# Kernel optimization log

Measured on AMD Instinct MI355X. Metric: run time of the kernel, lower is better.

The kernel has to match this reference:

```python
import jax, jax.numpy as jnp
import numpy as np

EPS = 1e-12
TAU = 1.0

def _normalize(x, axis=-1):
    # matches torch.nn.functional.normalize (p=2, eps=1e-12)
    n = jnp.linalg.norm(x, axis=axis, keepdims=True)
    return x / jnp.maximum(n, EPS)

def setup_inputs() -> dict:
    key = jax.random.key(0)
    ks = jax.random.split(key, 6)
    N, B, D, K = 8192, 512, 64, 4
    input_rating = jax.random.uniform(ks[0], (B, N), dtype=jnp.float32)
    # row-normalized-scale adjacency (mimics a normalized item-item graph)
    item_adj = jax.random.uniform(ks[1], (N, N), dtype=jnp.float32) * (2.0 / N)
    item_emb = jax.random.normal(ks[2], (N, D), dtype=jnp.float32) * float(np.sqrt(2.0 / (N + D)))
    proto_emb = jax.random.normal(ks[3], (K, D), dtype=jnp.float32) * float(np.sqrt(2.0 / (K + D)))
    enc_w = jax.random.normal(ks[4], (2 * D, N), dtype=jnp.float32) * float(np.sqrt(2.0 / (N + 2 * D)))
    enc_b = jax.random.normal(ks[5], (2 * D,), dtype=jnp.float32) * 0.01
    return {"input_rating": input_rating, "item_adj": item_adj, "item_emb": item_emb,
            "proto_emb": proto_emb, "enc_w": enc_w, "enc_b": enc_b}

def reference(input_rating, item_adj, item_emb, proto_emb, enc_w, enc_b):
    D = enc_b.shape[0] // 2
    prototypes = _normalize(proto_emb)          # [K, D]
    items = _normalize(item_emb)                # [N, D]
    cates = jax.nn.softmax(items @ prototypes.T / TAU, axis=-1)  # [N, K] (eval: mode branch)
    # per-prototype masked ratings, vectorized over K: [K, B, N]
    x_k = input_rating[None, :, :] * cates.T[:, None, :]
    x_k = _normalize(x_k)                       # fn.normalize(x_k, p=2) over items dim
    # two-hop propagation through dense item-item adjacency
    tmp = jnp.einsum('kbn,nm->kbm', x_k, item_adj)
    tmp = jnp.einsum('kbn,nm->kbm', tmp, item_adj)
    x = (tmp + x_k) / 2.0                       # dropout is identity in eval
    h = jnp.einsum('kbn,on->kbo', x, enc_w) + enc_b  # [K, B, 2D]
    mu = _normalize(h[..., :D])                 # [K, B, D]
    logvar = -h[..., D:]                        # [K, B, D]
    z = _normalize(mu)                          # eval: reparameterize returns mu
    logits_k = jnp.einsum('kbd,nd->kbn', z, items) / TAU
    probs = jnp.sum(jnp.exp(logits_k) * cates.T[:, None, :], axis=0)  # [B, N]
    logits = jnp.log(probs)
    return logits, mu, logvar
```

## Files before the change

kernel.cpp:

```cpp
#include <hip/hip_runtime.h>

typedef __attribute__((ext_vector_type(8))) short short8;
typedef __attribute__((ext_vector_type(4))) float f32x4;

#define AS3P(x) ((__attribute__((address_space(3))) void*)(x))
#define AS1P(x) ((const __attribute__((address_space(1))) void*)(x))

__device__ __forceinline__ unsigned short f2bf(float f) {
    unsigned int u = __float_as_uint(f);
    u += 0x7fffu + ((u >> 16) & 1u);
    return (unsigned short)(u >> 16);
}
__device__ __forceinline__ float bf2f(unsigned short b) {
    return __uint_as_float(((unsigned int)b) << 16);
}
__device__ __forceinline__ float waveReduceSum(float v) {
    #pragma unroll
    for (int off = 32; off; off >>= 1) v += __shfl_xor(v, off, 64);
    return v;
}

__global__ __launch_bounds__(256) void k_mega(const float* __restrict__ adj,
                                              unsigned short* __restrict__ adj_bf,
                                              const float* __restrict__ enc_w,
                                              unsigned short* __restrict__ encw,
                                              const float* __restrict__ item_emb,
                                              const float* __restrict__ proto,
                                              unsigned short* __restrict__ items_bf,
                                              float* __restrict__ catesT) {
    __shared__ float sp[256];
    int bx = blockIdx.x, tid = threadIdx.x;
    if (bx < 33280) {
        const float* src = (bx < 32768) ? adj : enc_w;
        unsigned short* dst = (bx < 32768) ? adj_bf : encw;
        size_t base = (bx < 32768) ? (size_t)bx : (size_t)(bx - 32768);
        size_t i = (base * 256 + tid) * 8;
        float4 a = *(const float4*)(src + i);
        float4 b = *(const float4*)(src + i + 4);
        uint4 pk;
        pk.x = (unsigned int)f2bf(a.x) | ((unsigned int)f2bf(a.y) << 16);
        pk.y = (unsigned int)f2bf(a.z) | ((unsigned int)f2bf(a.w) << 16);
        pk.z = (unsigned int)f2bf(b.x) | ((unsigned int)f2bf(b.y) << 16);
        pk.w = (unsigned int)f2bf(b.z) | ((unsigned int)f2bf(b.w) << 16);
        *(uint4*)(dst + i) = pk;
        return;
    }
    sp[tid] = proto[tid];
    __syncthreads();
    {
        float v = sp[tid];
        float ss = waveReduceSum(v * v);
        sp[tid] = v * (1.f / fmaxf(sqrtf(ss), 1e-12f));
    }
    __syncthreads();
    int i = (bx - 33280) * 256 + tid;
    const float4* row = (const float4*)(item_emb + (size_t)i * 64);
    float4 f[16];
    float ss = 0.f;
    #pragma unroll
    for (int q = 0; q < 16; ++q) {
        f[q] = row[q];
        ss += f[q].x * f[q].x + f[q].y * f[q].y + f[q].z * f[q].z + f[q].w * f[q].w;
    }
    float inv = 1.f / fmaxf(sqrtf(ss), 1e-12f);
    float dots[4] = {0.f, 0.f, 0.f, 0.f};
    unsigned short* ob = items_bf + (size_t)i * 64;
    #pragma unroll
    for (int q = 0; q < 16; ++q) {
        f[q].x *= inv; f[q].y *= inv; f[q].z *= inv; f[q].w *= inv;
        #pragma unroll
        for (int k = 0; k < 4; ++k) {
            dots[k] += f[q].x * sp[k * 64 + q * 4 + 0] + f[q].y * sp[k * 64 + q * 4 + 1]
                     + f[q].z * sp[k * 64 + q * 4 + 2] + f[q].w * sp[k * 64 + q * 4 + 3];
        }
    }
    #pragma unroll
    for (int q = 0; q < 16; q += 2) {
        uint4 pk;
        pk.x = (unsigned int)f2bf(f[q].x)     | ((unsigned int)f2bf(f[q].y) << 16);
        pk.y = (unsigned int)f2bf(f[q].z)     | ((unsigned int)f2bf(f[q].w) << 16);
        pk.z = (unsigned int)f2bf(f[q + 1].x) | ((unsigned int)f2bf(f[q + 1].y) << 16);
        pk.w = (unsigned int)f2bf(f[q + 1].z) | ((unsigned int)f2bf(f[q + 1].w) << 16);
        *(uint4*)(ob + q * 4) = pk;
    }
    float m = fmaxf(fmaxf(dots[0], dots[1]), fmaxf(dots[2], dots[3]));
    float e0 = expf(dots[0] - m), e1 = expf(dots[1] - m), e2 = expf(dots[2] - m), e3 = expf(dots[3] - m);
    float is = 1.f / (e0 + e1 + e2 + e3);
    catesT[0 * 8192 + i] = e0 * is;
    catesT[1 * 8192 + i] = e1 * is;
    catesT[2 * 8192 + i] = e2 * is;
    catesT[3 * 8192 + i] = e3 * is;
}

__global__ __launch_bounds__(256) void k_gemm_part(const unsigned short* __restrict__ A,
                                                   const unsigned short* __restrict__ B,
                                                   unsigned short* __restrict__ Cout,
                                                   int M, int ksplit, int lda, int ldb, int ldc) {
    __shared__ unsigned short lA[128 * 64];
    __shared__ unsigned short lB[128 * 64];
    int tid = threadIdx.x;
    int lane = tid & 63;
    int w = tid >> 6;
    int wr = w >> 1, wc = w & 1;
    int mBase = blockIdx.y * 128;
    int nBase = blockIdx.x * 128;
    int Kbeg = blockIdx.z * ksplit;
    int Kend = Kbeg + ksplit;

    f32x4 acc[4][4] = {};

    const unsigned short* Ablk = A + (size_t)mBase * lda;
    const unsigned short* Bblk = B + (size_t)nBase * ldb;
    int srow = tid >> 3;
    int scg = (tid & 7) ^ (srow & 7);
    char* ldsA_w = (char*)lA + w * 1024;
    char* ldsB_w = (char*)lB + w * 1024;

    for (int k0 = Kbeg; k0 < Kend; k0 += 64) {
        __syncthreads();
        #pragma unroll
        for (int it = 0; it < 4; ++it) {
            const unsigned short* ga = Ablk + (size_t)(it * 32 + srow) * lda + k0 + scg * 8;
            __builtin_amdgcn_global_load_lds(AS1P(ga), AS3P(ldsA_w + it * 4096), 16, 0, 0);
            const unsigned short* gb = Bblk + (size_t)(it * 32 + srow) * ldb + k0 + scg * 8;
            __builtin_amdgcn_global_load_lds(AS1P(gb), AS3P(ldsB_w + it * 4096), 16, 0, 0);
        }
        __syncthreads();
        #pragma unroll
        for (int kk = 0; kk < 2; ++kk) {
            short8 af[4], bfr[4];
            #pragma unroll
            for (int i = 0; i < 4; ++i) {
                int rowa = wr * 64 + i * 16 + (lane & 15);
                int slot = kk * 4 + (lane >> 4);
                af[i] = *(const short8*)((const char*)lA + rowa * 128 + ((slot ^ (rowa & 7)) * 16));
                int rowb = wc * 64 + i * 16 + (lane & 15);
                bfr[i] = *(const short8*)((const char*)lB + rowb * 128 + ((slot ^ (rowb & 7)) * 16));
            }
            #pragma unroll
            for (int i = 0; i < 4; ++i)
                #pragma unroll
                for (int j = 0; j < 4; ++j)
                    acc[i][j] = __builtin_amdgcn_mfma_f32_16x16x32_bf16(af[i], bfr[j], acc[i][j], 0, 0, 0);
        }
    }

    unsigned short* outP = Cout + (size_t)blockIdx.z * M * ldc;
    #pragma unroll
    for (int i = 0; i < 4; ++i) {
        int rbase = mBase + wr * 64 + i * 16 + (lane >> 4) * 4;
        #pragma unroll
        for (int j = 0; j < 4; ++j) {
            int col = nBase + wc * 64 + j * 16 + (lane & 15);
            #pragma unroll
            for (int r = 0; r < 4; ++r)
                outP[(size_t)(rbase + r) * ldc + col] = f2bf(acc[i][j][r]);
        }
    }
}

__global__ __launch_bounds__(256) void k_red1(const unsigned short* __restrict__ part,
                                              unsigned short* __restrict__ outT,
                                              const float* __restrict__ rating,
                                              const float* __restrict__ catesT,
                                              unsigned short* __restrict__ rating_bf,
                                              float* __restrict__ inv4) {
    __shared__ float t[64 * 129];
    int tid = threadIdx.x;
    if (blockIdx.x < 128) {
        int m0 = blockIdx.x * 64;
        #pragma unroll
        for (int j = 0; j < 4; ++j) {
            int f = tid + j * 256;
            int m = f >> 4, o = (f & 15) * 8;
            float a[8] = {0.f,0.f,0.f,0.f,0.f,0.f,0.f,0.f};
            #pragma unroll
            for (int sp = 0; sp < 16; ++sp) {
                const unsigned short* p = part + (size_t)sp * 8192 * 128 + (size_t)(m0 + m) * 128 + o;
                uint4 v = *(const uint4*)p;
                a[0] += bf2f((unsigned short)(v.x & 0xffff)); a[1] += bf2f((unsigned short)(v.x >> 16));
                a[2] += bf2f((unsigned short)(v.y & 0xffff)); a[3] += bf2f((unsigned short)(v.y >> 16));
                a[4] += bf2f((unsigned short)(v.z & 0xffff)); a[5] += bf2f((unsigned short)(v.z >> 16));
                a[6] += bf2f((unsigned short)(v.w & 0xffff)); a[7] += bf2f((unsigned short)(v.w >> 16));
            }
            #pragma unroll
            for (int e = 0; e < 8; ++e) t[m * 129 + o + e] = a[e];
        }
        __syncthreads();
        #pragma unroll
        for (int j = 0; j < 16; ++j) {
            int idx = tid + j * 256;
            int o = idx >> 5, mp = idx & 31;
            float v0 = t[(mp * 2 + 0) * 129 + o];
            float v1 = t[(mp * 2 + 1) * 129 + o];
            unsigned int pk = (unsigned int)f2bf(v0) | ((unsigned int)f2bf(v1) << 16);
            *(unsigned int*)(outT + (size_t)o * 8192 + m0 + mp * 2) = pk;
        }
        return;
    }
    int b = blockIdx.x - 128;
    const float* row = rating + (size_t)b * 8192;
    float s0 = 0.f, s1 = 0.f, s2 = 0.f, s3 = 0.f;
    #pragma unroll
    for (int j = 0; j < 8; ++j) {
        int i4 = tid + j * 256;
        float4 r = *(const float4*)(row + i4 * 4);
        ushort4 pk;
        pk.x = f2bf(r.x); pk.y = f2bf(r.y); pk.z = f2bf(r.z); pk.w = f2bf(r.w);
        *(ushort4*)(rating_bf + (size_t)b * 8192 + i4 * 4) = pk;
        float4 c0 = *(const float4*)(catesT + 0 * 8192 + i4 * 4);
        float4 c1 = *(const float4*)(catesT + 1 * 8192 + i4 * 4);
        float4 c2 = *(const float4*)(catesT + 2 * 8192 + i4 * 4);
        float4 c3 = *(const float4*)(catesT + 3 * 8192 + i4 * 4);
        float px, py, pz, pw;
        px = r.x * c0.x; py = r.y * c0.y; pz = r.z * c0.z; pw = r.w * c0.w;
        s0 += px * px + py * py + pz * pz + pw * pw;
        px = r.x * c1.x; py = r.y * c1.y; pz = r.z * c1.z; pw = r.w * c1.w;
        s1 += px * px + py * py + pz * pz + pw * pw;
        px = r.x * c2.x; py = r.y * c2.y; pz = r.z * c2.z; pw = r.w * c2.w;
        s2 += px * px + py * py + pz * pz + pw * pw;
        px = r.x * c3.x; py = r.y * c3.y; pz = r.z * c3.z; pw = r.w * c3.w;
        s3 += px * px + py * py + pz * pz + pw * pw;
    }
    s0 = waveReduceSum(s0); s1 = waveReduceSum(s1);
    s2 = waveReduceSum(s2); s3 = waveReduceSum(s3);
    if ((tid & 63) == 0) {
        int w = tid >> 6;
        t[w * 4 + 0] = s0; t[w * 4 + 1] = s1; t[w * 4 + 2] = s2; t[w * 4 + 3] = s3;
    }
    __syncthreads();
    if (tid < 4) {
        float ss = t[0 * 4 + tid] + t[1 * 4 + tid] + t[2 * 4 + tid] + t[3 * 4 + tid];
        inv4[b * 4 + tid] = 1.f / fmaxf(sqrtf(ss), 1e-12f);
    }
}

__global__ __launch_bounds__(256) void k_reduce_TG(const unsigned short* __restrict__ part,
                                                   const float* __restrict__ enc_w,
                                                   const float* __restrict__ catesT,
                                                   unsigned short* __restrict__ G) {
    __shared__ float t[64 * 129];
    int m0 = blockIdx.x * 64;
    int tid = threadIdx.x;
    #pragma unroll
    for (int j = 0; j < 4; ++j) {
        int f = tid + j * 256;
        int m = f >> 4, o = (f & 15) * 8;
        float a[8] = {0.f,0.f,0.f,0.f,0.f,0.f,0.f,0.f};
        #pragma unroll
        for (int sp = 0; sp < 16; ++sp) {
            const unsigned short* p = part + (size_t)sp * 8192 * 128 + (size_t)(m0 + m) * 128 + o;
            uint4 v = *(const uint4*)p;
            a[0] += bf2f((unsigned short)(v.x & 0xffff)); a[1] += bf2f((unsigned short)(v.x >> 16));
            a[2] += bf2f((unsigned short)(v.y & 0xffff)); a[3] += bf2f((unsigned short)(v.y >> 16));
            a[4] += bf2f((unsigned short)(v.z & 0xffff)); a[5] += bf2f((unsigned short)(v.z >> 16));
            a[6] += bf2f((unsigned short)(v.w & 0xffff)); a[7] += bf2f((unsigned short)(v.w >> 16));
        }
        #pragma unroll
        for (int e = 0; e < 8; ++e) t[m * 129 + o + e] = a[e];
    }
    __syncthreads();
    #pragma unroll
    for (int j = 0; j < 16; ++j) {
        int idx = tid + j * 256;
        int o = idx >> 5, mp = idx & 31;
        int m = m0 + mp * 2;
        float v0 = t[(mp * 2 + 0) * 129 + o];
        float v1 = t[(mp * 2 + 1) * 129 + o];
        v0 = 0.5f * (v0 + enc_w[(size_t)o * 8192 + m + 0]);
        v1 = 0.5f * (v1 + enc_w[(size_t)o * 8192 + m + 1]);
        #pragma unroll
        for (int k = 0; k < 4; ++k) {
            float c0 = catesT[(size_t)k * 8192 + m + 0];
            float c1 = catesT[(size_t)k * 8192 + m + 1];
            unsigned int pk = (unsigned int)f2bf(v0 * c0) | ((unsigned int)f2bf(v1 * c1) << 16);
            *(unsigned int*)(G + (size_t)(k * 128 + o) * 8192 + m) = pk;
        }
    }
}

__global__ __launch_bounds__(128) void k_reduce_h2(const unsigned short* __restrict__ hpart,
                                                   const float* __restrict__ enc_b,
                                                   const float* __restrict__ inv4,
                                                   unsigned short* __restrict__ mu_bf,
                                                   float* __restrict__ outp) {
    int r = blockIdx.x;
    int k = r >> 9, b = r & 511;
    int o = threadIdx.x;
    float s = 0.f;
    #pragma unroll
    for (int sp = 0; sp < 16; ++sp)
        s += bf2f(hpart[(size_t)sp * 262144 + (size_t)b * 512 + k * 128 + o]);
    s = s * inv4[b * 4 + k] + enc_b[o];
    const size_t MU0 = (size_t)512 * 8192;
    const size_t LV0 = MU0 + (size_t)2048 * 64;
    if (o < 64) {
        float ss = s * s;
        #pragma unroll
        for (int off = 32; off; off >>= 1) ss += __shfl_xor(ss, off, 64);
        float inv = 1.f / fmaxf(sqrtf(ss), 1e-12f);
        float mv = s * inv;
        outp[MU0 + (size_t)r * 64 + o] = mv;
        mu_bf[(size_t)r * 64 + o] = f2bf(mv);
    } else {
        outp[LV0 + (size_t)r * 64 + (o - 64)] = -s;
    }
}

__global__ __launch_bounds__(256) void k_logits_mfma(const unsigned short* __restrict__ mu_bf,
                                                     const unsigned short* __restrict__ items_bf,
                                                     const float* __restrict__ catesT,
                                                     float* __restrict__ out) {
    __shared__ unsigned short lA[128 * 64];
    __shared__ unsigned short lB[128 * 64];
    int tid = threadIdx.x;
    int lane = tid & 63, w = tid >> 6, wr = w >> 1, wc = w & 1;
    int nBase = blockIdx.x * 128, bBase = blockIdx.y * 128;
    int srow = tid >> 3;
    int scg = (tid & 7) ^ (srow & 7);
    char* ldsA_w = (char*)lA + w * 1024;
    char* ldsB_w = (char*)lB + w * 1024;

    #pragma unroll
    for (int it = 0; it < 4; ++it) {
        const unsigned short* gb = items_bf + (size_t)(nBase + it * 32 + srow) * 64 + scg * 8;
        __builtin_amdgcn_global_load_lds(AS1P(gb), AS3P(ldsB_w + it * 4096), 16, 0, 0);
    }

    f32x4 p[4][4] = {};
    for (int k = 0; k < 4; ++k) {
        __syncthreads();
        #pragma unroll
        for (int it = 0; it < 4; ++it) {
            const unsigned short* ga = mu_bf + (size_t)(k * 512 + bBase + it * 32 + srow) * 64 + scg * 8;
            __builtin_amdgcn_global_load_lds(AS1P(ga), AS3P(ldsA_w + it * 4096), 16, 0, 0);
        }
        __syncthreads();
        f32x4 acc[4][4] = {};
        #pragma unroll
        for (int kk = 0; kk < 2; ++kk) {
            short8 af[4], bfr[4];
            #pragma unroll
            for (int i = 0; i < 4; ++i) {
                int rowa = wr * 64 + i * 16 + (lane & 15);
                int slot = kk * 4 + (lane >> 4);
                af[i] = *(const short8*)((const char*)lA + rowa * 128 + ((slot ^ (rowa & 7)) * 16));
                int rowb = wc * 64 + i * 16 + (lane & 15);
                bfr[i] = *(const short8*)((const char*)lB + rowb * 128 + ((slot ^ (rowb & 7)) * 16));
            }
            #pragma unroll
            for (int i = 0; i < 4; ++i)
                #pragma unroll
                for (int j = 0; j < 4; ++j)
                    acc[i][j] = __builtin_amdgcn_mfma_f32_16x16x32_bf16(af[i], bfr[j], acc[i][j], 0, 0, 0);
        }
        #pragma unroll
        for (int j = 0; j < 4; ++j) {
            int col = nBase + wc * 64 + j * 16 + (lane & 15);
            float c = catesT[(size_t)k * 8192 + col];
            #pragma unroll
            for (int i = 0; i < 4; ++i)
                #pragma unroll
                for (int r = 0; r < 4; ++r)
                    p[i][j][r] += __expf(acc[i][j][r]) * c;
        }
    }
    #pragma unroll
    for (int i = 0; i < 4; ++i) {
        int rbase = bBase + wr * 64 + i * 16 + (lane >> 4) * 4;
        #pragma unroll
        for (int j = 0; j < 4; ++j) {
            int col = nBase + wc * 64 + j * 16 + (lane & 15);
            #pragma unroll
            for (int r = 0; r < 4; ++r)
                out[(size_t)(rbase + r) * 8192 + col] = __logf(p[i][j][r]);
        }
    }
}

extern "C" void kernel_launch(void* const* d_in, const int* in_sizes, int n_in,
                              void* d_out, int out_size, void* d_ws, size_t ws_size,
                              hipStream_t stream) {
    const float* rating   = (const float*)d_in[0];
    const float* adj      = (const float*)d_in[1];
    const float* item_emb = (const float*)d_in[2];
    const float* proto    = (const float*)d_in[3];
    const float* enc_w    = (const float*)d_in[4];
    const float* enc_b    = (const float*)d_in[5];
    float* out = (float*)d_out;

    char* ws = (char*)d_ws;
    unsigned short* adj_bf    = (unsigned short*)ws;
    unsigned short* part_bf   = adj_bf + (size_t)8192 * 8192;
    unsigned short* rating_bf = part_bf + (size_t)16 * 8192 * 128;
    unsigned short* G         = rating_bf + (size_t)512 * 8192;
    unsigned short* W1T       = G + (size_t)512 * 8192;
    unsigned short* encw      = W1T + (size_t)128 * 8192;
    unsigned short* hpart     = encw + (size_t)128 * 8192;
    unsigned short* items_bf  = hpart + (size_t)16 * 512 * 512;
    unsigned short* mu_bf     = items_bf + (size_t)8192 * 64;
    float* catesT = (float*)(mu_bf + (size_t)2048 * 64);
    float* inv4   = catesT + (size_t)4 * 8192;

    k_mega<<<33312, 256, 0, stream>>>(adj, adj_bf, enc_w, encw, item_emb, proto, items_bf, catesT);

    k_gemm_part<<<dim3(1, 64, 16), 256, 0, stream>>>(adj_bf, encw, part_bf, 8192, 512, 8192, 8192, 128);
    k_red1<<<640, 256, 0, stream>>>(part_bf, W1T, rating, catesT, rating_bf, inv4);

    k_gemm_part<<<dim3(1, 64, 16), 256, 0, stream>>>(adj_bf, W1T, part_bf, 8192, 512, 8192, 8192, 128);
    k_reduce_TG<<<128, 256, 0, stream>>>(part_bf, enc_w, catesT, G);

    k_gemm_part<<<dim3(4, 4, 16), 256, 0, stream>>>(rating_bf, G, hpart, 512, 512, 8192, 8192, 512);
    k_reduce_h2<<<2048, 128, 0, stream>>>(hpart, enc_b, inv4, mu_bf, out);

    k_logits_mfma<<<dim3(64, 4), 256, 0, stream>>>(mu_bf, items_bf, catesT, out);
}
```

Measured before the change: 207.5 us.

## Fuse fp32-to-bf16 adjacency conversion into GEMM A-tile loads

Drops the standalone pass that converted the 8192x8192 fp32 adjacency to bf16. A new GEMM kernel loads fp32 A tiles straight into LDS and converts them to bf16 in registers before the MFMA. This removes the separate read-and-write of the whole adjacency and its bf16 workspace buffer. In exchange, each of the two propagation GEMMs now reads twice as many bytes of A, needs a larger LDS footprint, and adds conversion work to the inner loop.

Result: slower. 223.7 us (+7.8%).

```diff
diff --git a/kernel.cpp b/kernel.cpp
--- a/kernel.cpp
+++ b/kernel.cpp
@@ -14,15 +14,16 @@
 __device__ __forceinline__ float bf2f(unsigned short b) {
     return __uint_as_float(((unsigned int)b) << 16);
 }
+__device__ __forceinline__ unsigned int pk2bf(float a, float b) {
+    return (unsigned int)f2bf(a) | ((unsigned int)f2bf(b) << 16);
+}
 __device__ __forceinline__ float waveReduceSum(float v) {
     #pragma unroll
     for (int off = 32; off; off >>= 1) v += __shfl_xor(v, off, 64);
     return v;
 }
 
-__global__ __launch_bounds__(256) void k_mega(const float* __restrict__ adj,
-                                              unsigned short* __restrict__ adj_bf,
-                                              const float* __restrict__ enc_w,
+__global__ __launch_bounds__(256) void k_prep(const float* __restrict__ enc_w,
                                               unsigned short* __restrict__ encw,
                                               const float* __restrict__ item_emb,
                                               const float* __restrict__ proto,
@@ -30,19 +31,14 @@
                                               float* __restrict__ catesT) {
     __shared__ float sp[256];
     int bx = blockIdx.x, tid = threadIdx.x;
-    if (bx < 33280) {
-        const float* src = (bx < 32768) ? adj : enc_w;
-        unsigned short* dst = (bx < 32768) ? adj_bf : encw;
-        size_t base = (bx < 32768) ? (size_t)bx : (size_t)(bx - 32768);
-        size_t i = (base * 256 + tid) * 8;
-        float4 a = *(const float4*)(src + i);
-        float4 b = *(const float4*)(src + i + 4);
+    if (bx < 512) {
+        size_t i = ((size_t)bx * 256 + tid) * 8;
+        float4 a = *(const float4*)(enc_w + i);
+        float4 b = *(const float4*)(enc_w + i + 4);
         uint4 pk;
-        pk.x = (unsigned int)f2bf(a.x) | ((unsigned int)f2bf(a.y) << 16);
-        pk.y = (unsigned int)f2bf(a.z) | ((unsigned int)f2bf(a.w) << 16);
-        pk.z = (unsigned int)f2bf(b.x) | ((unsigned int)f2bf(b.y) << 16);
-        pk.w = (unsigned int)f2bf(b.z) | ((unsigned int)f2bf(b.w) << 16);
-        *(uint4*)(dst + i) = pk;
+        pk.x = pk2bf(a.x, a.y); pk.y = pk2bf(a.z, a.w);
+        pk.z = pk2bf(b.x, b.y); pk.w = pk2bf(b.z, b.w);
+        *(uint4*)(encw + i) = pk;
         return;
     }
     sp[tid] = proto[tid];
@@ -53,7 +49,7 @@
         sp[tid] = v * (1.f / fmaxf(sqrtf(ss), 1e-12f));
     }
     __syncthreads();
-    int i = (bx - 33280) * 256 + tid;
+    int i = (bx - 512) * 256 + tid;
     const float4* row = (const float4*)(item_emb + (size_t)i * 64);
     float4 f[16];
     float ss = 0.f;
@@ -77,10 +73,8 @@
     #pragma unroll
     for (int q = 0; q < 16; q += 2) {
         uint4 pk;
-        pk.x = (unsigned int)f2bf(f[q].x)     | ((unsigned int)f2bf(f[q].y) << 16);
-        pk.y = (unsigned int)f2bf(f[q].z)     | ((unsigned int)f2bf(f[q].w) << 16);
-        pk.z = (unsigned int)f2bf(f[q + 1].x) | ((unsigned int)f2bf(f[q + 1].y) << 16);
-        pk.w = (unsigned int)f2bf(f[q + 1].z) | ((unsigned int)f2bf(f[q + 1].w) << 16);
+        pk.x = pk2bf(f[q].x, f[q].y);         pk.y = pk2bf(f[q].z, f[q].w);
+        pk.z = pk2bf(f[q + 1].x, f[q + 1].y); pk.w = pk2bf(f[q + 1].z, f[q + 1].w);
         *(uint4*)(ob + q * 4) = pk;
     }
     float m = fmaxf(fmaxf(dots[0], dots[1]), fmaxf(dots[2], dots[3]));
@@ -90,6 +84,85 @@
     catesT[1 * 8192 + i] = e1 * is;
     catesT[2 * 8192 + i] = e2 * is;
     catesT[3 * 8192 + i] = e3 * is;
+}
+
+__global__ __launch_bounds__(256) void k_gemm_f32A(const float* __restrict__ A,
+                                                   const unsigned short* __restrict__ B,
+                                                   unsigned short* __restrict__ Cout,
+                                                   int ksplit) {
+    __shared__ float lAf[128 * 64];
+    __shared__ unsigned short lB[128 * 64];
+    int tid = threadIdx.x;
+    int lane = tid & 63;
+    int w = tid >> 6;
+    int wr = w >> 1, wc = w & 1;
+    int mBase = blockIdx.y * 128;
+    int Kbeg = blockIdx.z * ksplit;
+    int Kend = Kbeg + ksplit;
+
+    f32x4 acc[4][4] = {};
+
+    const float* Ablk = A + (size_t)mBase * 8192;
+    int arow_l = w * 4 + (lane >> 4);
+    int aq = lane & 15;
+    int acol = (aq ^ arow_l) * 4;
+    int srow = tid >> 3;
+    int scg = (tid & 7) ^ (srow & 7);
+    char* ldsA_w = (char*)lAf + w * 1024;
+    char* ldsB_w = (char*)lB + w * 1024;
+
+    for (int k0 = Kbeg; k0 < Kend; k0 += 64) {
+        __syncthreads();
+        #pragma unroll
+        for (int it = 0; it < 8; ++it) {
+            int row = it * 16 + arow_l;
+            const float* ga = Ablk + (size_t)row * 8192 + k0 + acol;
+            __builtin_amdgcn_global_load_lds(AS1P(ga), AS3P(ldsA_w + it * 4096), 16, 0, 0);
+        }
+        #pragma unroll
+        for (int it = 0; it < 4; ++it) {
+            const unsigned short* gb = B + (size_t)(it * 32 + srow) * 8192 + k0 + scg * 8;
+            __builtin_amdgcn_global_load_lds(AS1P(gb), AS3P(ldsB_w + it * 4096), 16, 0, 0);
+        }
+        __syncthreads();
+        #pragma unroll
+        for (int kk = 0; kk < 2; ++kk) {
+            short8 af[4], bfr[4];
+            #pragma unroll
+            for (int i = 0; i < 4; ++i) {
+                int rowa = wr * 64 + i * 16 + (lane & 15);
+                int slot = kk * 4 + (lane >> 4);
+                const char* pbase = (const char*)lAf + rowa * 256;
+                int q0 = (2 * slot) ^ (rowa & 15);
+                float4 fa = *(const float4*)(pbase + q0 * 16);
+                float4 fb = *(const float4*)(pbase + (q0 ^ 1) * 16);
+                union { unsigned int u[4]; short8 s; } cv;
+                cv.u[0] = pk2bf(fa.x, fa.y); cv.u[1] = pk2bf(fa.z, fa.w);
+                cv.u[2] = pk2bf(fb.x, fb.y); cv.u[3] = pk2bf(fb.z, fb.w);
+                af[i] = cv.s;
+                int rowb = wc * 64 + i * 16 + (lane & 15);
+                bfr[i] = *(const short8*)((const char*)lB + rowb * 128 + ((slot ^ (rowb & 7)) * 16));
+            }
+            #pragma unroll
+            for (int i = 0; i < 4; ++i)
+                #pragma unroll
+                for (int j = 0; j < 4; ++j)
+                    acc[i][j] = __builtin_amdgcn_mfma_f32_16x16x32_bf16(af[i], bfr[j], acc[i][j], 0, 0, 0);
+        }
+    }
+
+    unsigned short* outP = Cout + (size_t)blockIdx.z * 8192 * 128;
+    #pragma unroll
+    for (int i = 0; i < 4; ++i) {
+        int rbase = mBase + wr * 64 + i * 16 + (lane >> 4) * 4;
+        #pragma unroll
+        for (int j = 0; j < 4; ++j) {
+            int col = wc * 64 + j * 16 + (lane & 15);
+            #pragma unroll
+            for (int r = 0; r < 4; ++r)
+                outP[(size_t)(rbase + r) * 128 + col] = f2bf(acc[i][j][r]);
+        }
+    }
 }
 
 __global__ __launch_bounds__(256) void k_gemm_part(const unsigned short* __restrict__ A,
@@ -193,8 +266,7 @@
             int o = idx >> 5, mp = idx & 31;
             float v0 = t[(mp * 2 + 0) * 129 + o];
             float v1 = t[(mp * 2 + 1) * 129 + o];
-            unsigned int pk = (unsigned int)f2bf(v0) | ((unsigned int)f2bf(v1) << 16);
-            *(unsigned int*)(outT + (size_t)o * 8192 + m0 + mp * 2) = pk;
+            *(unsigned int*)(outT + (size_t)o * 8192 + m0 + mp * 2) = pk2bf(v0, v1);
         }
         return;
     }
@@ -273,8 +345,7 @@
         for (int k = 0; k < 4; ++k) {
             float c0 = catesT[(size_t)k * 8192 + m + 0];
             float c1 = catesT[(size_t)k * 8192 + m + 1];
-            unsigned int pk = (unsigned int)f2bf(v0 * c0) | ((unsigned int)f2bf(v1 * c1) << 16);
-            *(unsigned int*)(G + (size_t)(k * 128 + o) * 8192 + m) = pk;
+            *(unsigned int*)(G + (size_t)(k * 128 + o) * 8192 + m) = pk2bf(v0 * c0, v1 * c1);
         }
     }
 }
@@ -390,8 +461,7 @@
     float* out = (float*)d_out;
 
     char* ws = (char*)d_ws;
-    unsigned short* adj_bf    = (unsigned short*)ws;
-    unsigned short* part_bf   = adj_bf + (size_t)8192 * 8192;
+    unsigned short* part_bf   = (unsigned short*)ws;
     unsigned short* rating_bf = part_bf + (size_t)16 * 8192 * 128;
     unsigned short* G         = rating_bf + (size_t)512 * 8192;
     unsigned short* W1T       = G + (size_t)512 * 8192;
@@ -402,12 +472,12 @@
     float* catesT = (float*)(mu_bf + (size_t)2048 * 64);
     float* inv4   = catesT + (size_t)4 * 8192;
 
-    k_mega<<<33312, 256, 0, stream>>>(adj, adj_bf, enc_w, encw, item_emb, proto, items_bf, catesT);
-
-    k_gemm_part<<<dim3(1, 64, 16), 256, 0, stream>>>(adj_bf, encw, part_bf, 8192, 512, 8192, 8192, 128);
+    k_prep<<<544, 256, 0, stream>>>(enc_w, encw, item_emb, proto, items_bf, catesT);
+
+    k_gemm_f32A<<<dim3(1, 64, 16), 256, 0, stream>>>(adj, encw, part_bf, 512);
     k_red1<<<640, 256, 0, stream>>>(part_bf, W1T, rating, catesT, rating_bf, inv4);
 
-    k_gemm_part<<<dim3(1, 64, 16), 256, 0, stream>>>(adj_bf, W1T, part_bf, 8192, 512, 8192, 8192, 128);
+    k_gemm_f32A<<<dim3(1, 64, 16), 256, 0, stream>>>(adj, W1T, part_bf, 512);
     k_reduce_TG<<<128, 256, 0, stream>>>(part_bf, enc_w, catesT, G);
 
     k_gemm_part<<<dim3(4, 4, 16), 256, 0, stream>>>(rating_bf, G, hpart, 512, 512, 8192, 8192, 512);
```

## Swap GEMM operand roles to emit W1T/G directly, drop LDS transposes

Applied to the files above, without the earlier changes.

The two adjacency GEMMs are re-launched with encw/W1T as the A operand and adj_bf as B, so the split-K partials come out already in [128, 8192] transposed layout. The reduce kernels then become simple elementwise sums with vectorized loads and stores, with no shared-memory transpose. The third GEMM also doubles its split-K factor to 32 with half the K per split, which gives more blocks but doubles the partial traffic reduced in k_reduce_h2. Whether the GEMM is as efficient with the swapped operands depends on how k_gemm_part reads A and B.

Measured after the change: 199.3 us. 3.9% less time.

```diff
diff --git a/kernel.cpp b/kernel.cpp
--- a/kernel.cpp
+++ b/kernel.cpp
@@ -13,6 +13,9 @@
 }
 __device__ __forceinline__ float bf2f(unsigned short b) {
     return __uint_as_float(((unsigned int)b) << 16);
+}
+__device__ __forceinline__ unsigned int pk2bf(float a, float b) {
+    return (unsigned int)f2bf(a) | ((unsigned int)f2bf(b) << 16);
 }
 __device__ __forceinline__ float waveReduceSum(float v) {
     #pragma unroll
@@ -38,10 +41,8 @@
         float4 a = *(const float4*)(src + i);
         float4 b = *(const float4*)(src + i + 4);
         uint4 pk;
-        pk.x = (unsigned int)f2bf(a.x) | ((unsigned int)f2bf(a.y) << 16);
-        pk.y = (unsigned int)f2bf(a.z) | ((unsigned int)f2bf(a.w) << 16);
-        pk.z = (unsigned int)f2bf(b.x) | ((unsigned int)f2bf(b.y) << 16);
-        pk.w = (unsigned int)f2bf(b.z) | ((unsigned int)f2bf(b.w) << 16);
+        pk.x = pk2bf(a.x, a.y); pk.y = pk2bf(a.z, a.w);
+        pk.z = pk2bf(b.x, b.y); pk.w = pk2bf(b.z, b.w);
         *(uint4*)(dst + i) = pk;
         return;
     }
@@ -77,10 +78,8 @@
     #pragma unroll
     for (int q = 0; q < 16; q += 2) {
         uint4 pk;
-        pk.x = (unsigned int)f2bf(f[q].x)     | ((unsigned int)f2bf(f[q].y) << 16);
-        pk.y = (unsigned int)f2bf(f[q].z)     | ((unsigned int)f2bf(f[q].w) << 16);
-        pk.z = (unsigned int)f2bf(f[q + 1].x) | ((unsigned int)f2bf(f[q + 1].y) << 16);
-        pk.w = (unsigned int)f2bf(f[q + 1].z) | ((unsigned int)f2bf(f[q + 1].w) << 16);
+        pk.x = pk2bf(f[q].x, f[q].y);         pk.y = pk2bf(f[q].z, f[q].w);
+        pk.z = pk2bf(f[q + 1].x, f[q + 1].y); pk.w = pk2bf(f[q + 1].z, f[q + 1].w);
         *(uint4*)(ob + q * 4) = pk;
     }
     float m = fmaxf(fmaxf(dots[0], dots[1]), fmaxf(dots[2], dots[3]));
@@ -159,46 +158,32 @@
     }
 }
 
-__global__ __launch_bounds__(256) void k_red1(const unsigned short* __restrict__ part,
-                                              unsigned short* __restrict__ outT,
+__global__ __launch_bounds__(256) void k_redW(const unsigned short* __restrict__ part,
+                                              unsigned short* __restrict__ W1T,
                                               const float* __restrict__ rating,
                                               const float* __restrict__ catesT,
                                               unsigned short* __restrict__ rating_bf,
                                               float* __restrict__ inv4) {
-    __shared__ float t[64 * 129];
     int tid = threadIdx.x;
-    if (blockIdx.x < 128) {
-        int m0 = blockIdx.x * 64;
-        #pragma unroll
-        for (int j = 0; j < 4; ++j) {
-            int f = tid + j * 256;
-            int m = f >> 4, o = (f & 15) * 8;
-            float a[8] = {0.f,0.f,0.f,0.f,0.f,0.f,0.f,0.f};
-            #pragma unroll
-            for (int sp = 0; sp < 16; ++sp) {
-                const unsigned short* p = part + (size_t)sp * 8192 * 128 + (size_t)(m0 + m) * 128 + o;
-                uint4 v = *(const uint4*)p;
-                a[0] += bf2f((unsigned short)(v.x & 0xffff)); a[1] += bf2f((unsigned short)(v.x >> 16));
-                a[2] += bf2f((unsigned short)(v.y & 0xffff)); a[3] += bf2f((unsigned short)(v.y >> 16));
-                a[4] += bf2f((unsigned short)(v.z & 0xffff)); a[5] += bf2f((unsigned short)(v.z >> 16));
-                a[6] += bf2f((unsigned short)(v.w & 0xffff)); a[7] += bf2f((unsigned short)(v.w >> 16));
-            }
-            #pragma unroll
-            for (int e = 0; e < 8; ++e) t[m * 129 + o + e] = a[e];
-        }
-        __syncthreads();
-        #pragma unroll
-        for (int j = 0; j < 16; ++j) {
-            int idx = tid + j * 256;
-            int o = idx >> 5, mp = idx & 31;
-            float v0 = t[(mp * 2 + 0) * 129 + o];
-            float v1 = t[(mp * 2 + 1) * 129 + o];
-            unsigned int pk = (unsigned int)f2bf(v0) | ((unsigned int)f2bf(v1) << 16);
-            *(unsigned int*)(outT + (size_t)o * 8192 + m0 + mp * 2) = pk;
-        }
+    if (blockIdx.x < 512) {
+        size_t base = ((size_t)blockIdx.x * 256 + tid) * 8;
+        float a[8] = {0.f,0.f,0.f,0.f,0.f,0.f,0.f,0.f};
+        #pragma unroll
+        for (int sp = 0; sp < 16; ++sp) {
+            uint4 v = *(const uint4*)(part + (size_t)sp * 1048576 + base);
+            a[0] += bf2f((unsigned short)(v.x & 0xffff)); a[1] += bf2f((unsigned short)(v.x >> 16));
+            a[2] += bf2f((unsigned short)(v.y & 0xffff)); a[3] += bf2f((unsigned short)(v.y >> 16));
+            a[4] += bf2f((unsigned short)(v.z & 0xffff)); a[5] += bf2f((unsigned short)(v.z >> 16));
+            a[6] += bf2f((unsigned short)(v.w & 0xffff)); a[7] += bf2f((unsigned short)(v.w >> 16));
+        }
+        uint4 pk;
+        pk.x = pk2bf(a[0], a[1]); pk.y = pk2bf(a[2], a[3]);
+        pk.z = pk2bf(a[4], a[5]); pk.w = pk2bf(a[6], a[7]);
+        *(uint4*)(W1T + base) = pk;
         return;
     }
-    int b = blockIdx.x - 128;
+    __shared__ float t[16];
+    int b = blockIdx.x - 512;
     const float* row = rating + (size_t)b * 8192;
     float s0 = 0.f, s1 = 0.f, s2 = 0.f, s3 = 0.f;
     #pragma unroll
@@ -235,47 +220,36 @@
     }
 }
 
-__global__ __launch_bounds__(256) void k_reduce_TG(const unsigned short* __restrict__ part,
-                                                   const float* __restrict__ enc_w,
-                                                   const float* __restrict__ catesT,
-                                                   unsigned short* __restrict__ G) {
-    __shared__ float t[64 * 129];
-    int m0 = blockIdx.x * 64;
-    int tid = threadIdx.x;
-    #pragma unroll
-    for (int j = 0; j < 4; ++j) {
-        int f = tid + j * 256;
-        int m = f >> 4, o = (f & 15) * 8;
-        float a[8] = {0.f,0.f,0.f,0.f,0.f,0.f,0.f,0.f};
-        #pragma unroll
-        for (int sp = 0; sp < 16; ++sp) {
-            const unsigned short* p = part + (size_t)sp * 8192 * 128 + (size_t)(m0 + m) * 128 + o;
-            uint4 v = *(const uint4*)p;
-            a[0] += bf2f((unsigned short)(v.x & 0xffff)); a[1] += bf2f((unsigned short)(v.x >> 16));
-            a[2] += bf2f((unsigned short)(v.y & 0xffff)); a[3] += bf2f((unsigned short)(v.y >> 16));
-            a[4] += bf2f((unsigned short)(v.z & 0xffff)); a[5] += bf2f((unsigned short)(v.z >> 16));
-            a[6] += bf2f((unsigned short)(v.w & 0xffff)); a[7] += bf2f((unsigned short)(v.w >> 16));
-        }
-        #pragma unroll
-        for (int e = 0; e < 8; ++e) t[m * 129 + o + e] = a[e];
-    }
-    __syncthreads();
-    #pragma unroll
-    for (int j = 0; j < 16; ++j) {
-        int idx = tid + j * 256;
-        int o = idx >> 5, mp = idx & 31;
-        int m = m0 + mp * 2;
-        float v0 = t[(mp * 2 + 0) * 129 + o];
-        float v1 = t[(mp * 2 + 1) * 129 + o];
-        v0 = 0.5f * (v0 + enc_w[(size_t)o * 8192 + m + 0]);
-        v1 = 0.5f * (v1 + enc_w[(size_t)o * 8192 + m + 1]);
-        #pragma unroll
-        for (int k = 0; k < 4; ++k) {
-            float c0 = catesT[(size_t)k * 8192 + m + 0];
-            float c1 = catesT[(size_t)k * 8192 + m + 1];
-            unsigned int pk = (unsigned int)f2bf(v0 * c0) | ((unsigned int)f2bf(v1 * c1) << 16);
-            *(unsigned int*)(G + (size_t)(k * 128 + o) * 8192 + m) = pk;
-        }
+__global__ __launch_bounds__(256) void k_red_G(const unsigned short* __restrict__ part,
+                                               const float* __restrict__ enc_w,
+                                               const float* __restrict__ catesT,
+                                               unsigned short* __restrict__ G) {
+    size_t base = ((size_t)blockIdx.x * 256 + threadIdx.x) * 8;
+    int o = (int)(base >> 13);
+    int n = (int)(base & 8191);
+    float a[8] = {0.f,0.f,0.f,0.f,0.f,0.f,0.f,0.f};
+    #pragma unroll
+    for (int sp = 0; sp < 16; ++sp) {
+        uint4 v = *(const uint4*)(part + (size_t)sp * 1048576 + base);
+        a[0] += bf2f((unsigned short)(v.x & 0xffff)); a[1] += bf2f((unsigned short)(v.x >> 16));
+        a[2] += bf2f((unsigned short)(v.y & 0xffff)); a[3] += bf2f((unsigned short)(v.y >> 16));
+        a[4] += bf2f((unsigned short)(v.z & 0xffff)); a[5] += bf2f((unsigned short)(v.z >> 16));
+        a[6] += bf2f((unsigned short)(v.w & 0xffff)); a[7] += bf2f((unsigned short)(v.w >> 16));
+    }
+    float4 e0 = *(const float4*)(enc_w + base);
+    float4 e1 = *(const float4*)(enc_w + base + 4);
+    a[0] = 0.5f * (a[0] + e0.x); a[1] = 0.5f * (a[1] + e0.y);
+    a[2] = 0.5f * (a[2] + e0.z); a[3] = 0.5f * (a[3] + e0.w);
+    a[4] = 0.5f * (a[4] + e1.x); a[5] = 0.5f * (a[5] + e1.y);
+    a[6] = 0.5f * (a[6] + e1.z); a[7] = 0.5f * (a[7] + e1.w);
+    #pragma unroll
+    for (int k = 0; k < 4; ++k) {
+        float4 c0 = *(const float4*)(catesT + (size_t)k * 8192 + n);
+        float4 c1 = *(const float4*)(catesT + (size_t)k * 8192 + n + 4);
+        uint4 pk;
+        pk.x = pk2bf(a[0] * c0.x, a[1] * c0.y); pk.y = pk2bf(a[2] * c0.z, a[3] * c0.w);
+        pk.z = pk2bf(a[4] * c1.x, a[5] * c1.y); pk.w = pk2bf(a[6] * c1.z, a[7] * c1.w);
+        *(uint4*)(G + (size_t)(k * 128 + o) * 8192 + n) = pk;
     }
 }
 
@@ -289,7 +263,7 @@
     int o = threadIdx.x;
     float s = 0.f;
     #pragma unroll
-    for (int sp = 0; sp < 16; ++sp)
+    for (int sp = 0; sp < 32; ++sp)
         s += bf2f(hpart[(size_t)sp * 262144 + (size_t)b * 512 + k * 128 + o]);
     s = s * inv4[b * 4 + k] + enc_b[o];
     const size_t MU0 = (size_t)512 * 8192;
@@ -392,25 +366,25 @@
     char* ws = (char*)d_ws;
     unsigned short* adj_bf    = (unsigned short*)ws;
     unsigned short* part_bf   = adj_bf + (size_t)8192 * 8192;
-    unsigned short* rating_bf = part_bf + (size_t)16 * 8192 * 128;
+    unsigned short* rating_bf = part_bf + (size_t)16 * 1048576;
     unsigned short* G         = rating_bf + (size_t)512 * 8192;
     unsigned short* W1T       = G + (size_t)512 * 8192;
     unsigned short* encw      = W1T + (size_t)128 * 8192;
     unsigned short* hpart     = encw + (size_t)128 * 8192;
-    unsigned short* items_bf  = hpart + (size_t)16 * 512 * 512;
+    unsigned short* items_bf  = hpart + (size_t)32 * 262144;
     unsigned short* mu_bf     = items_bf + (size_t)8192 * 64;
     float* catesT = (float*)(mu_bf + (size_t)2048 * 64);
     float* inv4   = catesT + (size_t)4 * 8192;
 
     k_mega<<<33312, 256, 0, stream>>>(adj, adj_bf, enc_w, encw, item_emb, proto, items_bf, catesT);
 
-    k_gemm_part<<<dim3(1, 64, 16), 256, 0, stream>>>(adj_bf, encw, part_bf, 8192, 512, 8192, 8192, 128);
-    k_red1<<<640, 256, 0, stream>>>(part_bf, W1T, rating, catesT, rating_bf, inv4);
-
-    k_gemm_part<<<dim3(1, 64, 16), 256, 0, stream>>>(adj_bf, W1T, part_bf, 8192, 512, 8192, 8192, 128);
-    k_reduce_TG<<<128, 256, 0, stream>>>(part_bf, enc_w, catesT, G);
-
-    k_gemm_part<<<dim3(4, 4, 16), 256, 0, stream>>>(rating_bf, G, hpart, 512, 512, 8192, 8192, 512);
+    k_gemm_part<<<dim3(64, 1, 16), 256, 0, stream>>>(encw, adj_bf, part_bf, 128, 512, 8192, 8192, 8192);
+    k_redW<<<1024, 256, 0, stream>>>(part_bf, W1T, rating, catesT, rating_bf, inv4);
+
+    k_gemm_part<<<dim3(64, 1, 16), 256, 0, stream>>>(W1T, adj_bf, part_bf, 128, 512, 8192, 8192, 8192);
+    k_red_G<<<512, 256, 0, stream>>>(part_bf, enc_w, catesT, G);
+
+    k_gemm_part<<<dim3(4, 4, 32), 256, 0, stream>>>(rating_bf, G, hpart, 512, 256, 8192, 8192, 512);
     k_reduce_h2<<<2048, 128, 0, stream>>>(hpart, enc_b, inv4, mu_bf, out);
 
     k_logits_mfma<<<dim3(64, 4), 256, 0, stream>>>(mu_bf, items_bf, catesT, out);
```
